# Kernel optimization log

Measured on AMD Instinct MI355X. Metric: run time of the kernel, lower is better.

Reference implementation:

```python
import jax, jax.numpy as jnp
import numpy as np

D_MODEL = 1024; D_STATE = 64; D_CONV = 4; EXPAND = 2; HEADDIM = 128; NGROUPS = 1; CHUNK = 256
D_INNER = EXPAND * D_MODEL            # 2048
NHEADS = D_INNER // HEADDIM           # 16
CONV_DIM = D_INNER + 2 * NGROUPS * D_STATE   # 2176
D_IN_PROJ = 2 * D_INNER + 2 * NGROUPS * D_STATE + NHEADS  # 4240
B = 4; G = 256; L = 2048
EPS = 1e-5


def setup_inputs() -> dict:
    key = jax.random.key(0)
    ks = jax.random.split(key, 12)
    def nrm(k, shape, s=0.02):
        return jax.random.normal(k, shape, jnp.float32) * s
    return dict(
        local_repr=jax.random.normal(ks[0], (B, L, D_MODEL), jnp.float32),
        global_repr=jax.random.normal(ks[1], (B, G, D_MODEL), jnp.float32),
        norm1_w=jnp.ones((D_MODEL,), jnp.float32), norm1_b=jnp.zeros((D_MODEL,), jnp.float32),
        norm2_w=jnp.ones((D_MODEL,), jnp.float32), norm2_b=jnp.zeros((D_MODEL,), jnp.float32),
        norm3_w=jnp.ones((D_MODEL,), jnp.float32), norm3_b=jnp.zeros((D_MODEL,), jnp.float32),
        in_proj_w=nrm(ks[2], (D_IN_PROJ, D_MODEL)),
        conv_w=nrm(ks[3], (CONV_DIM, D_CONV), 0.2),
        conv_b=jnp.zeros((CONV_DIM,), jnp.float32),
        dt_bias=jnp.log(jnp.expm1(jax.random.uniform(ks[4], (NHEADS,), jnp.float32, 1e-3, 0.1))),
        A_log=jnp.log(jax.random.uniform(ks[5], (NHEADS,), jnp.float32, 1.0, 16.0)),
        D_skip=jnp.ones((NHEADS,), jnp.float32),
        ssd_norm_w=jnp.ones((D_INNER,), jnp.float32),
        out_proj_w=nrm(ks[6], (D_MODEL, D_INNER)),
        ffn_w1=nrm(ks[7], (D_MODEL // 2, D_MODEL)),
        ffn_b1=jnp.zeros((D_MODEL // 2,), jnp.float32),
        ffn_w2=nrm(ks[8], (D_MODEL, D_MODEL // 2)),
        ffn_b2=jnp.zeros((D_MODEL,), jnp.float32),
    )


def _ln(x, w, b):
    mu = jnp.mean(x, axis=-1, keepdims=True)
    var = jnp.mean((x - mu) ** 2, axis=-1, keepdims=True)
    return (x - mu) * jax.lax.rsqrt(var + EPS) * w + b


def _segsum(a):
    # a: (..., T) -> (..., T, T) lower-triangular sums a[j+1..i]
    T = a.shape[-1]
    cs = jnp.cumsum(a, axis=-1)
    diff = cs[..., :, None] - cs[..., None, :]
    mask = jnp.tril(jnp.ones((T, T), bool))
    return jnp.where(mask, diff, -jnp.inf)


def _ssd(xdt, a_dt, Bh, Ch):
    # xdt: (b,t,h,p) = x*dt ; a_dt: (b,t,h) = dt*A ; Bh,Ch: (b,t,h,n)
    b, t, h, p = xdt.shape
    n = Bh.shape[-1]
    c = t // CHUNK
    X = xdt.reshape(b, c, CHUNK, h, p)
    Bc = Bh.reshape(b, c, CHUNK, h, n)
    Cc = Ch.reshape(b, c, CHUNK, h, n)
    Ac = a_dt.reshape(b, c, CHUNK, h).transpose(0, 3, 1, 2)  # (b,h,c,k)
    A_cum = jnp.cumsum(Ac, axis=-1)
    Lm = jnp.exp(_segsum(Ac))                                # (b,h,c,k,k)
    Y_diag = jnp.einsum('bckhn,bcshn,bhcks,bcshp->bckhp', Cc, Bc, Lm, X)
    decay_states = jnp.exp(A_cum[..., -1:] - A_cum)          # (b,h,c,k)
    states = jnp.einsum('bckhn,bhck,bckhp->bchpn', Bc, decay_states, X)
    A_last = jnp.pad(A_cum[..., -1], ((0, 0), (0, 0), (1, 0)))
    decay_chunk = jnp.exp(_segsum(A_last))                   # (b,h,c+1,c+1)
    states = jnp.concatenate([jnp.zeros_like(states[:, :1]), states], axis=1)
    new_states = jnp.einsum('bhzc,bchpn->bzhpn', decay_chunk, states)
    states_in = new_states[:, :-1]                           # (b,c,h,p,n)
    out_decay = jnp.exp(A_cum)                               # (b,h,c,k)
    Y_off = jnp.einsum('bckhn,bchpn,bhck->bckhp', Cc, states_in, out_decay)
    return (Y_diag + Y_off).reshape(b, t, h, p)


def _mamba2(x, in_proj_w, conv_w, conv_b, dt_bias, A_log, D_skip, ssd_norm_w, out_proj_w):
    b, t, _ = x.shape
    zxbcdt = x @ in_proj_w.T                                  # (b,t,D_IN_PROJ)
    z = zxbcdt[..., :D_INNER]
    xBC = zxbcdt[..., D_INNER:D_INNER + CONV_DIM]
    dt = jax.nn.softplus(zxbcdt[..., D_INNER + CONV_DIM:] + dt_bias)  # (b,t,h)
    # causal depthwise conv1d, kernel D_CONV
    xp = jnp.pad(xBC, ((0, 0), (D_CONV - 1, 0), (0, 0)))
    xBC = sum(xp[:, i:i + t, :] * conv_w[:, i] for i in range(D_CONV)) + conv_b
    xBC = jax.nn.silu(xBC)
    xs = xBC[..., :D_INNER].reshape(b, t, NHEADS, HEADDIM)
    Bm = xBC[..., D_INNER:D_INNER + NGROUPS * D_STATE].reshape(b, t, NGROUPS, D_STATE)
    Cm = xBC[..., D_INNER + NGROUPS * D_STATE:].reshape(b, t, NGROUPS, D_STATE)
    rep = NHEADS // NGROUPS
    Bh = jnp.repeat(Bm, rep, axis=2)
    Ch = jnp.repeat(Cm, rep, axis=2)
    A = -jnp.exp(A_log)                                       # (h,)
    Y = _ssd(xs * dt[..., None], dt * A, Bh, Ch)
    y = Y + D_skip[None, None, :, None] * xs
    y = y.reshape(b, t, D_INNER)
    # gated RMSNorm (norm_before_gate=False)
    y = y * jax.nn.silu(z)
    y = y * jax.lax.rsqrt(jnp.mean(y * y, axis=-1, keepdims=True) + EPS) * ssd_norm_w
    return y @ out_proj_w.T


def reference(local_repr, global_repr, norm1_w, norm1_b, norm2_w, norm2_b, norm3_w, norm3_b,
              in_proj_w, conv_w, conv_b, dt_bias, A_log, D_skip, ssd_norm_w, out_proj_w,
              ffn_w1, ffn_b1, ffn_w2, ffn_b2):
    local_n = _ln(local_repr, norm1_w, norm1_b)
    global_n = _ln(global_repr, norm2_w, norm2_b)
    x = jnp.concatenate([global_n, local_n], axis=1)          # (B, G+L, D)
    x = _mamba2(x, in_proj_w, conv_w, conv_b, dt_bias, A_log, D_skip, ssd_norm_w, out_proj_w)
    x = x[:, -local_n.shape[1]:, :] + local_n
    x = _ln(x, norm3_w, norm3_b)
    h = jax.nn.gelu(x @ ffn_w1.T + ffn_b1, approximate=False)
    return (h @ ffn_w2.T + ffn_b2) + x
```

## Files before the change

### kernel.cpp

```cpp
#include <hip/hip_runtime.h>
#include <math.h>

#define B_ 4
#define L_ 2048
#define G_ 256
#define T_ 2304
#define DM 1024
#define DINNER 2048
#define NH 16
#define HD 128
#define NSTATE 64
#define CONVD 2176
#define DPROJ 4240
#define NPROJ_PAD 4352
#define NCHUNK 9
#define CK 256
#define EPSV 1e-5f
#define CROWS 16

typedef unsigned short bf16t;
using bf16x8 = __attribute__((ext_vector_type(8))) short;
using f32x4  = __attribute__((ext_vector_type(4))) float;

__device__ __forceinline__ float bf2f(bf16t u) {
  return __uint_as_float(((unsigned int)u) << 16);
}
__device__ __forceinline__ bf16t f2bf(float f) {
  unsigned int u = __float_as_uint(f);
  u += 0x7FFFu + ((u >> 16) & 1u);
  return (bf16t)(u >> 16);
}

__device__ __forceinline__ void g2lds16(const bf16t* g, short* l) {
  __builtin_amdgcn_global_load_lds(
      (const __attribute__((address_space(1))) unsigned int*)g,
      (__attribute__((address_space(3))) unsigned int*)l, 16, 0, 0);
}

__device__ __forceinline__ float2 block_reduce2(float a, float b) {
  __shared__ float sa[4], sb[4];
  #pragma unroll
  for (int off = 32; off > 0; off >>= 1) {
    a += __shfl_down(a, off, 64);
    b += __shfl_down(b, off, 64);
  }
  int lane = threadIdx.x & 63, wid = threadIdx.x >> 6;
  if (lane == 0) { sa[wid] = a; sb[wid] = b; }
  __syncthreads();
  return make_float2(sa[0] + sa[1] + sa[2] + sa[3], sb[0] + sb[1] + sb[2] + sb[3]);
}

__global__ __launch_bounds__(256) void ln_cvt_kernel(
    const float* __restrict__ localr, const float* __restrict__ globalr,
    const float* __restrict__ w1, const float* __restrict__ b1,
    const float* __restrict__ w2, const float* __restrict__ b2,
    bf16t* __restrict__ x, const float* __restrict__ inpw,
    bf16t* __restrict__ inpw_bf) {
  int blk = blockIdx.x;
  if (blk < B_ * T_) {
    int t = blk % T_, b = blk / T_;
    const float *src, *w, *bb;
    if (t < G_) { src = globalr + ((long)b * G_ + t) * DM;        w = w2; bb = b2; }
    else        { src = localr  + ((long)b * L_ + (t - G_)) * DM; w = w1; bb = b1; }
    int d = threadIdx.x * 4;
    float4 v = *(const float4*)&src[d];
    float s = v.x + v.y + v.z + v.w;
    float sq = v.x * v.x + v.y * v.y + v.z * v.z + v.w * v.w;
    float2 r2 = block_reduce2(s, sq);
    float mu = r2.x * (1.f / DM);
    float var = r2.y * (1.f / DM) - mu * mu;
    float rstd = rsqrtf(var + EPSV);
    float4 wv = *(const float4*)&w[d];
    float4 bv = *(const float4*)&bb[d];
    ushort4 o;
    o.x = f2bf((v.x - mu) * rstd * wv.x + bv.x);
    o.y = f2bf((v.y - mu) * rstd * wv.y + bv.y);
    o.z = f2bf((v.z - mu) * rstd * wv.z + bv.z);
    o.w = f2bf((v.w - mu) * rstd * wv.w + bv.w);
    *(ushort4*)&x[(long)blk * DM + d] = o;
  } else {
    long i = (long)(blk - B_ * T_) * 1024 + threadIdx.x * 4;
    const long nreal = (long)DPROJ * DM, ntot = (long)NPROJ_PAD * DM;
    if (i < ntot) {
      ushort4 o = {0, 0, 0, 0};
      if (i < nreal) {
        float4 v = *(const float4*)&inpw[i];
        o.x = f2bf(v.x); o.y = f2bf(v.y); o.z = f2bf(v.z); o.w = f2bf(v.w);
      }
      *(ushort4*)&inpw_bf[i] = o;
    }
  }
}

template<int EPI, bool OFFS>
__global__ __launch_bounds__(256) void gemm_mfma(
    const bf16t* __restrict__ A, const bf16t* __restrict__ W,
    const float* __restrict__ bias, const bf16t* __restrict__ res,
    float* __restrict__ Cf, bf16t* __restrict__ Cb,
    bf16t* __restrict__ z, bf16t* __restrict__ xpre, float* __restrict__ dtr,
    int N, int K) {
  __shared__ __align__(16) short LDS[128 * 136];
  short* As = LDS;
  short* Ws = LDS + 128 * 32;
  int tid = threadIdx.x;
  int lane = tid & 63, w = tid >> 6;
  int wr = w >> 1, wc = w & 1;
  int bm = blockIdx.y * 128, bn = blockIdx.x * 128;
  long bmA = OFFS ? ((long)(bm >> 11) * T_ + G_ + (bm & 2047)) : (long)bm;

  int r1 = tid >> 2,         s1 = (((tid & 3) ^ ((r1 >> 1) & 3))) * 8;
  int r2 = (tid + 256) >> 2, s2 = (((tid & 3) ^ ((r2 >> 1) & 3))) * 8;
  const bf16t* gA1 = A + (bmA + r1) * K + s1;
  const bf16t* gA2 = A + (bmA + r2) * K + s2;
  const bf16t* gW1 = W + (long)(bn + r1) * K + s1;
  const bf16t* gW2 = W + (long)(bn + r2) * K + s2;
  short* lA1 = As + tid * 8;
  short* lA2 = As + (tid + 256) * 8;
  short* lW1 = Ws + tid * 8;
  short* lW2 = Ws + (tid + 256) * 8;

  int arow = wr * 64 + (lane & 15);
  int brow = wc * 64 + (lane & 15);
  int koff = (((lane >> 4) ^ (((lane & 15) >> 1) & 3))) * 8;

  f32x4 acc[4][4] = {};
  for (int k0 = 0; k0 < K; k0 += 32) {
    g2lds16(gA1 + k0, lA1);
    g2lds16(gA2 + k0, lA2);
    g2lds16(gW1 + k0, lW1);
    g2lds16(gW2 + k0, lW2);
    __syncthreads();
    bf16x8 af[4], bf[4];
    #pragma unroll
    for (int mi = 0; mi < 4; mi++) af[mi] = *(bf16x8*)&As[(arow + mi * 16) * 32 + koff];
    #pragma unroll
    for (int ni = 0; ni < 4; ni++) bf[ni] = *(bf16x8*)&Ws[(brow + ni * 16) * 32 + koff];
    #pragma unroll
    for (int mi = 0; mi < 4; mi++)
      #pragma unroll
      for (int ni = 0; ni < 4; ni++)
        acc[mi][ni] = __builtin_amdgcn_mfma_f32_16x16x32_bf16(af[mi], bf[ni], acc[mi][ni], 0, 0, 0);
    __syncthreads();
  }

  int rb = wr * 64 + (lane >> 4) * 4;
  int cb = wc * 64 + (lane & 15);

  if (EPI == 0 && bn >= DINNER + CONVD) {
    #pragma unroll
    for (int mi = 0; mi < 4; mi++)
      #pragma unroll
      for (int ni = 0; ni < 4; ni++)
        #pragma unroll
        for (int r = 0; r < 4; r++) {
          int col = cb + ni * 16;
          if (col < NH)
            dtr[(long)(bm + rb + mi * 16 + r) * NH + col] = acc[mi][ni][r];
        }
    return;
  }

  if (EPI == 3) {
    float* Cs32 = (float*)LDS;
    #pragma unroll
    for (int pass = 0; pass < 2; pass++) {
      __syncthreads();
      if (wr == pass) {
        #pragma unroll
        for (int mi = 0; mi < 4; mi++)
          #pragma unroll
          for (int ni = 0; ni < 4; ni++)
            #pragma unroll
            for (int r = 0; r < 4; r++) {
              int lrow = (lane >> 4) * 4 + mi * 16 + r;
              Cs32[lrow * 136 + cb + ni * 16] = acc[mi][ni][r];
            }
      }
      __syncthreads();
      #pragma unroll
      for (int q = 0; q < 4; q++) {
        int row = q * 16 + (tid >> 4);
        int col = (tid & 15) * 8;
        long grow = bm + pass * 64 + row; int gcol = bn + col;
        float4 v0 = *(float4*)&Cs32[row * 136 + col];
        float4 v1 = *(float4*)&Cs32[row * 136 + col + 4];
        float4 b0 = *(const float4*)&bias[gcol];
        float4 b1 = *(const float4*)&bias[gcol + 4];
        bf16x8 rv = *(const bf16x8*)&res[grow * N + gcol];
        v0.x += b0.x + bf2f((bf16t)rv[0]); v0.y += b0.y + bf2f((bf16t)rv[1]);
        v0.z += b0.z + bf2f((bf16t)rv[2]); v0.w += b0.w + bf2f((bf16t)rv[3]);
        v1.x += b1.x + bf2f((bf16t)rv[4]); v1.y += b1.y + bf2f((bf16t)rv[5]);
        v1.z += b1.z + bf2f((bf16t)rv[6]); v1.w += b1.w + bf2f((bf16t)rv[7]);
        *(float4*)&Cf[grow * N + gcol] = v0;
        *(float4*)&Cf[grow * N + gcol + 4] = v1;
      }
    }
    return;
  }

  __syncthreads();
  bf16t* Cs = (bf16t*)LDS;
  #pragma unroll
  for (int mi = 0; mi < 4; mi++)
    #pragma unroll
    for (int ni = 0; ni < 4; ni++)
      #pragma unroll
      for (int r = 0; r < 4; r++) {
        float v = acc[mi][ni][r];
        if (EPI == 2) {
          v += bias[bn + cb + ni * 16];
          v = 0.5f * v * (1.f + erff(v * 0.70710678118f));
        }
        Cs[(rb + mi * 16 + r) * 136 + cb + ni * 16] = f2bf(v);
      }
  __syncthreads();
  #pragma unroll
  for (int pass = 0; pass < 8; pass++) {
    int row = pass * 16 + (tid >> 4);
    int col = (tid & 15) * 8;
    bf16x8 vv = *(bf16x8*)&Cs[row * 136 + col];
    long grow = bm + row; int gcol = bn + col;
    if (EPI == 0) {
      if (bn < DINNER) *(bf16x8*)&z[grow * DINNER + gcol] = vv;
      else             *(bf16x8*)&xpre[grow * CONVD + (gcol - DINNER)] = vv;
    } else {
      *(bf16x8*)&Cb[grow * N + gcol] = vv;
    }
  }
}

__global__ __launch_bounds__(256) void cumsum_kernel(
    const float* __restrict__ dtraw, const float* __restrict__ dt_bias,
    const float* __restrict__ A_log, float* __restrict__ dt,
    float* __restrict__ Acum) {
  int bid = blockIdx.x;
  int c = bid % NCHUNK; int hh = bid / NCHUNK;
  int h = hh % NH; int b = hh / NH;
  int k = threadIdx.x;
  float a = -__expf(A_log[h]);
  long t = (long)b * T_ + c * CK + k;
  float v0 = dtraw[t * NH + h] + dt_bias[h];
  float dtv = (v0 > 20.f) ? v0 : log1pf(__expf(v0));
  dt[t * NH + h] = dtv;
  float v = dtv * a;
  __shared__ float buf[2][CK];
  int cur = 0;
  buf[0][k] = v; __syncthreads();
  for (int off = 1; off < CK; off <<= 1) {
    float tv = buf[cur][k];
    if (k >= off) tv += buf[cur][k - off];
    buf[1 - cur][k] = tv; cur ^= 1; __syncthreads();
  }
  Acum[(long)bid * CK + k] = buf[cur][k];
}

__global__ __launch_bounds__(256) void conv_kernel(
    const bf16t* __restrict__ xpre, const float* __restrict__ cw,
    const float* __restrict__ cb, bf16t* __restrict__ out) {
  int gt = blockIdx.x * 256 + threadIdx.x;
  int cg = gt % 272; int rt = gt / 272;
  int c0 = cg * 8;
  long r0 = (long)rt * CROWS;
  int t0 = (int)(r0 % T_);

  float wreg[4][8];
  #pragma unroll
  for (int j = 0; j < 8; j++) {
    float4 wa = *(const float4*)&cw[(c0 + j) * 4];
    wreg[0][j] = wa.x; wreg[1][j] = wa.y; wreg[2][j] = wa.z; wreg[3][j] = wa.w;
  }
  float4 cb0 = *(const float4*)&cb[c0];
  float4 cb1 = *(const float4*)&cb[c0 + 4];
  float bias[8] = {cb0.x, cb0.y, cb0.z, cb0.w, cb1.x, cb1.y, cb1.z, cb1.w};

  bf16x8 win[4];
  #pragma unroll
  for (int i = 0; i < 3; i++) {
    if (t0 - 3 + i >= 0) win[i] = *(const bf16x8*)&xpre[(r0 - 3 + i) * CONVD + c0];
    else                 win[i] = bf16x8{0,0,0,0,0,0,0,0};
  }

  #pragma unroll
  for (int k = 0; k < CROWS; k++) {
    win[3] = *(const bf16x8*)&xpre[(r0 + k) * CONVD + c0];
    float acc[8];
    #pragma unroll
    for (int j = 0; j < 8; j++) acc[j] = bias[j];
    #pragma unroll
    for (int i = 0; i < 4; i++)
      #pragma unroll
      for (int j = 0; j < 8; j++)
        acc[j] += bf2f((bf16t)win[i][j]) * wreg[i][j];
    bf16x8 o;
    #pragma unroll
    for (int j = 0; j < 8; j++) {
      float s = acc[j] / (1.f + __expf(-acc[j]));
      o[j] = (short)f2bf(s);
    }
    *(bf16x8*)&out[(r0 + k) * CONVD + c0] = o;
    win[0] = win[1]; win[1] = win[2]; win[2] = win[3];
  }
}

__global__ __launch_bounds__(256) void chunk_states_kernel(
    const bf16t* __restrict__ xbc, const float* __restrict__ dt,
    const float* __restrict__ Acum, float* __restrict__ cs) {
  int bid = blockIdx.x;
  int h = bid & 15; int bc = bid >> 4;
  int c = bc & 7; int b = bc >> 3;
  int tid = threadIdx.x;
  int lane = tid & 63, w = tid >> 6;
  long tch = (long)b * T_ + c * CK;
  int acb = ((b * NH + h) * NCHUNK + c) * CK;
  float Alast = Acum[acb + CK - 1];

  __shared__ bf16t Xt[128][72];
  __shared__ bf16t Bt[64][72];
  __shared__ float wk[64];

  f32x4 acc[8] = {};
  for (int kb = 0; kb < 4; kb++) {
    int s0 = kb * 64;
    __syncthreads();
    if (tid < 64)
      wk[tid] = __expf(Alast - Acum[acb + s0 + tid]) * dt[(tch + s0 + tid) * NH + h];
    __syncthreads();
    for (int e = tid; e < 64 * 32; e += 256) {
      int s = e & 63, p4 = e >> 6;
      ushort4 u = *(const ushort4*)&xbc[(tch + s0 + s) * CONVD + h * HD + p4 * 4];
      float wv = wk[s];
      Xt[p4 * 4 + 0][s] = f2bf(bf2f(u.x) * wv);
      Xt[p4 * 4 + 1][s] = f2bf(bf2f(u.y) * wv);
      Xt[p4 * 4 + 2][s] = f2bf(bf2f(u.z) * wv);
      Xt[p4 * 4 + 3][s] = f2bf(bf2f(u.w) * wv);
    }
    for (int e = tid; e < 64 * 16; e += 256) {
      int s = e & 63, n4 = e >> 6;
      ushort4 u = *(const ushort4*)&xbc[(tch + s0 + s) * CONVD + DINNER + n4 * 4];
      Bt[n4 * 4 + 0][s] = u.x; Bt[n4 * 4 + 1][s] = u.y;
      Bt[n4 * 4 + 2][s] = u.z; Bt[n4 * 4 + 3][s] = u.w;
    }
    __syncthreads();
    #pragma unroll
    for (int ks = 0; ks < 2; ks++) {
      int koff = (lane >> 4) * 8 + ks * 32;
      bf16x8 bfr = *(bf16x8*)&Bt[w * 16 + (lane & 15)][koff];
      #pragma unroll
      for (int mi = 0; mi < 8; mi++) {
        bf16x8 af = *(bf16x8*)&Xt[mi * 16 + (lane & 15)][koff];
        acc[mi] = __builtin_amdgcn_mfma_f32_16x16x32_bf16(af, bfr, acc[mi], 0, 0, 0);
      }
    }
  }
  int cbid = (b * NCHUNK + c) * NH + h;
  float* out = cs + (long)cbid * HD * NSTATE;
  int n = w * 16 + (lane & 15);
  #pragma unroll
  for (int mi = 0; mi < 8; mi++) {
    #pragma unroll
    for (int r = 0; r < 4; r++) {
      int p = mi * 16 + (lane >> 4) * 4 + r;
      out[p * NSTATE + n] = acc[mi][r];
    }
  }
}

__global__ __launch_bounds__(256) void state_pass_kernel(
    float* __restrict__ cs, const float* __restrict__ Acum) {
  int bh = blockIdx.x;
  int b = bh / NH, h = bh % NH;
  int e0 = blockIdx.y * 1024 + threadIdx.x;
  for (int q = 0; q < 4; q++) {
    int e = e0 + q * 256;
    float s = 0.f;
    for (int c = 0; c < NCHUNK; c++) {
      long idx = ((long)(b * NCHUNK + c) * NH + h) * (HD * NSTATE) + e;
      if (c < NCHUNK - 1) {
        float tmp = cs[idx];
        cs[idx] = s;
        float g = __expf(Acum[((b * NH + h) * NCHUNK + c) * CK + CK - 1]);
        s = s * g + tmp;
      } else {
        cs[idx] = s;
      }
    }
  }
}

__global__ __launch_bounds__(256) void ssd_y_kernel(
    const bf16t* __restrict__ xbc, const float* __restrict__ dt,
    const float* __restrict__ Acum, const float* __restrict__ sin_,
    const float* __restrict__ Dskip, bf16t* __restrict__ Y) {
  int bid = blockIdx.x;
  int h = bid & 15; int bc = bid >> 4;
  int c = 1 + (bc & 7); int b = bc >> 3;
  int rt = blockIdx.y;
  int tid = threadIdx.x;
  int lane = tid & 63, w = tid >> 6;
  int wr = w >> 1, wc = w & 1;
  long tch = (long)b * T_ + c * CK;
  long tbase = tch + rt * 128;
  int acb = ((b * NH + h) * NCHUNK + c) * CK;

  __shared__ bf16t Cs[128][72];
  __shared__ bf16t Bs[64][72];
  __shared__ bf16t Xt[128][72];
  __shared__ bf16t Sm[128][72];
  __shared__ float Akl[128];
  __shared__ float Asl[64];
  __shared__ float dts[64];

  for (int e = tid; e < 128 * 8; e += 256) {
    int row = e >> 3, seg = (e & 7) * 8;
    *(bf16x8*)&Cs[row][seg] =
        *(const bf16x8*)&xbc[(tbase + row) * CONVD + DINNER + NSTATE + seg];
  }
  if (tid < 128) Akl[tid] = Acum[acb + rt * 128 + tid];

  f32x4 acc[4][4] = {};
  int nsb = 2 * (rt + 1);
  for (int sb = 0; sb < nsb; sb++) {
    int s0 = sb * 64;
    __syncthreads();
    if (tid < 64) {
      Asl[tid] = Acum[acb + s0 + tid];
      dts[tid] = dt[(tch + s0 + tid) * NH + h];
    }
    __syncthreads();
    for (int e = tid; e < 64 * 8; e += 256) {
      int row = e >> 3, seg = (e & 7) * 8;
      *(bf16x8*)&Bs[row][seg] =
          *(const bf16x8*)&xbc[(tch + s0 + row) * CONVD + DINNER + seg];
    }
    for (int e = tid; e < 64 * 32; e += 256) {
      int s = e & 63, p4 = e >> 6;
      ushort4 u = *(const ushort4*)&xbc[(tch + s0 + s) * CONVD + h * HD + p4 * 4];
      float dtv = dts[s];
      Xt[p4 * 4 + 0][s] = f2bf(bf2f(u.x) * dtv);
      Xt[p4 * 4 + 1][s] = f2bf(bf2f(u.y) * dtv);
      Xt[p4 * 4 + 2][s] = f2bf(bf2f(u.z) * dtv);
      Xt[p4 * 4 + 3][s] = f2bf(bf2f(u.w) * dtv);
    }
    __syncthreads();
    {
      f32x4 sacc[2][4] = {};
      int rw0 = w * 32;
      #pragma unroll
      for (int ks = 0; ks < 2; ks++) {
        int koff = (lane >> 4) * 8 + ks * 32;
        bf16x8 a0 = *(bf16x8*)&Cs[rw0 + (lane & 15)][koff];
        bf16x8 a1 = *(bf16x8*)&Cs[rw0 + 16 + (lane & 15)][koff];
        #pragma unroll
        for (int ni = 0; ni < 4; ni++) {
          bf16x8 bfr = *(bf16x8*)&Bs[ni * 16 + (lane & 15)][koff];
          sacc[0][ni] = __builtin_amdgcn_mfma_f32_16x16x32_bf16(a0, bfr, sacc[0][ni], 0, 0, 0);
          sacc[1][ni] = __builtin_amdgcn_mfma_f32_16x16x32_bf16(a1, bfr, sacc[1][ni], 0, 0, 0);
        }
      }
      #pragma unroll
      for (int mi = 0; mi < 2; mi++) {
        #pragma unroll
        for (int ni = 0; ni < 4; ni++) {
          #pragma unroll
          for (int r = 0; r < 4; r++) {
            int row = rw0 + mi * 16 + (lane >> 4) * 4 + r;
            int scol = ni * 16 + (lane & 15);
            int kglob = rt * 128 + row;
            int sglob = s0 + scol;
            float val = 0.f;
            if (sglob <= kglob) val = sacc[mi][ni][r] * __expf(Akl[row] - Asl[scol]);
            Sm[row][scol] = f2bf(val);
          }
        }
      }
    }
    __syncthreads();
    #pragma unroll
    for (int ks = 0; ks < 2; ks++) {
      int koff = (lane >> 4) * 8 + ks * 32;
      bf16x8 af[4], bfr[4];
      #pragma unroll
      for (int mi = 0; mi < 4; mi++) af[mi] = *(bf16x8*)&Sm[wr * 64 + mi * 16 + (lane & 15)][koff];
      #pragma unroll
      for (int ni = 0; ni < 4; ni++) bfr[ni] = *(bf16x8*)&Xt[wc * 64 + ni * 16 + (lane & 15)][koff];
      #pragma unroll
      for (int mi = 0; mi < 4; mi++)
        #pragma unroll
        for (int ni = 0; ni < 4; ni++)
          acc[mi][ni] = __builtin_amdgcn_mfma_f32_16x16x32_bf16(af[mi], bfr[ni], acc[mi][ni], 0, 0, 0);
    }
  }

  float ekr[16];
  #pragma unroll
  for (int mi = 0; mi < 4; mi++)
    #pragma unroll
    for (int r = 0; r < 4; r++)
      ekr[mi * 4 + r] = __expf(Akl[wr * 64 + mi * 16 + (lane >> 4) * 4 + r]);

  int cbid = (b * NCHUNK + c) * NH + h;
  const float* sinb = sin_ + (long)cbid * HD * NSTATE;
  #pragma unroll
  for (int ni = 0; ni < 4; ni++) {
    f32x4 offacc[4] = {};
    int p = wc * 64 + ni * 16 + (lane & 15);
    #pragma unroll
    for (int ks = 0; ks < 2; ks++) {
      int koff = (lane >> 4) * 8 + ks * 32;
      const float* srow = sinb + p * NSTATE + koff;
      float4 sa = *(const float4*)srow;
      float4 sbv = *(const float4*)(srow + 4);
      bf16x8 bfr;
      bfr[0] = (short)f2bf(sa.x);  bfr[1] = (short)f2bf(sa.y);
      bfr[2] = (short)f2bf(sa.z);  bfr[3] = (short)f2bf(sa.w);
      bfr[4] = (short)f2bf(sbv.x); bfr[5] = (short)f2bf(sbv.y);
      bfr[6] = (short)f2bf(sbv.z); bfr[7] = (short)f2bf(sbv.w);
      #pragma unroll
      for (int mi = 0; mi < 4; mi++) {
        bf16x8 af = *(bf16x8*)&Cs[wr * 64 + mi * 16 + (lane & 15)][koff];
        offacc[mi] = __builtin_amdgcn_mfma_f32_16x16x32_bf16(af, bfr, offacc[mi], 0, 0, 0);
      }
    }
    #pragma unroll
    for (int mi = 0; mi < 4; mi++)
      #pragma unroll
      for (int r = 0; r < 4; r++)
        acc[mi][ni][r] += ekr[mi * 4 + r] * offacc[mi][r];
  }

  float dsk = Dskip[h];
  #pragma unroll
  for (int mi = 0; mi < 4; mi++) {
    #pragma unroll
    for (int r = 0; r < 4; r++) {
      int row = wr * 64 + mi * 16 + (lane >> 4) * 4 + r;
      long t = tbase + row;
      #pragma unroll
      for (int ni = 0; ni < 4; ni++) {
        int p = wc * 64 + ni * 16 + (lane & 15);
        float xsv = bf2f(xbc[t * CONVD + h * HD + p]);
        Y[t * DINNER + h * HD + p] = f2bf(acc[mi][ni][r] + dsk * xsv);
      }
    }
  }
}

__global__ __launch_bounds__(256) void gate_rms_cvt_kernel(
    const bf16t* __restrict__ z, const float* __restrict__ nw,
    bf16t* __restrict__ Y,
    const float* __restrict__ outw, const float* __restrict__ f1w,
    const float* __restrict__ f2w, bf16t* __restrict__ o_out,
    bf16t* __restrict__ o_f1, bf16t* __restrict__ o_f2) {
  int blk = blockIdx.x;
  if (blk < B_ * L_) {
    long r = (long)(blk >> 11) * T_ + G_ + (blk & 2047);
    const bf16t* zrow = z + r * DINNER;
    bf16t* yrow = Y + r * DINNER;
    int tid = threadIdx.x;
    float v[8]; float sq = 0.f;
    #pragma unroll
    for (int i = 0; i < 4; i++) {
      int d = tid * 2 + 512 * i;
      ushort2 zu = *(const ushort2*)&zrow[d];
      ushort2 yu = *(const ushort2*)&yrow[d];
      float z0 = bf2f(zu.x), z1 = bf2f(zu.y);
      float y0 = bf2f(yu.x) * (z0 / (1.f + __expf(-z0)));
      float y1 = bf2f(yu.y) * (z1 / (1.f + __expf(-z1)));
      v[2 * i] = y0; v[2 * i + 1] = y1;
      sq += y0 * y0 + y1 * y1;
    }
    float2 r2 = block_reduce2(sq, 0.f);
    float rms = rsqrtf(r2.x * (1.f / DINNER) + EPSV);
    #pragma unroll
    for (int i = 0; i < 4; i++) {
      int d = tid * 2 + 512 * i;
      ushort2 o;
      o.x = f2bf(v[2 * i] * rms * nw[d]);
      o.y = f2bf(v[2 * i + 1] * rms * nw[d + 1]);
      *(ushort2*)&yrow[d] = o;
    }
  } else {
    long i = (long)(blk - B_ * L_) * 1024 + threadIdx.x * 4;
    const long n1 = (long)DM * DINNER;
    const long n2 = (long)(DM / 2) * DM;
    const float* src; bf16t* dst; long off;
    if (i < n1) { src = outw; dst = o_out; off = i; }
    else if (i < n1 + n2) { src = f1w; dst = o_f1; off = i - n1; }
    else { src = f2w; dst = o_f2; off = i - n1 - n2; }
    float4 v = *(const float4*)&src[off];
    ushort4 o;
    o.x = f2bf(v.x); o.y = f2bf(v.y); o.z = f2bf(v.z); o.w = f2bf(v.w);
    *(ushort4*)&dst[off] = o;
  }
}

__global__ __launch_bounds__(256) void res_ln3_kernel(
    const bf16t* __restrict__ mfull, const bf16t* __restrict__ x,
    const float* __restrict__ w3, const float* __restrict__ b3,
    bf16t* __restrict__ x2) {
  int rl = blockIdx.x;
  int tl = rl & 2047, b = rl >> 11;
  long rt = (long)b * T_ + G_ + tl;
  const bf16t* m = mfull + (long)rl * DM;
  const bf16t* xr = x + rt * DM;
  int tid = threadIdx.x;
  float v[4]; float s = 0.f, sq = 0.f;
  #pragma unroll
  for (int i = 0; i < 2; i++) {
    int d = tid * 2 + 512 * i;
    ushort2 mu2 = *(const ushort2*)&m[d];
    ushort2 xu2 = *(const ushort2*)&xr[d];
    float a0 = bf2f(mu2.x) + bf2f(xu2.x);
    float a1 = bf2f(mu2.y) + bf2f(xu2.y);
    v[2 * i] = a0; v[2 * i + 1] = a1;
    s += a0 + a1; sq += a0 * a0 + a1 * a1;
  }
  float2 r2 = block_reduce2(s, sq);
  float mu = r2.x * (1.f / DM);
  float var = r2.y * (1.f / DM) - mu * mu;
  float rstd = rsqrtf(var + EPSV);
  bf16t* dst = x2 + (long)rl * DM;
  #pragma unroll
  for (int i = 0; i < 2; i++) {
    int d = tid * 2 + 512 * i;
    ushort2 o;
    o.x = f2bf((v[2 * i] - mu) * rstd * w3[d] + b3[d]);
    o.y = f2bf((v[2 * i + 1] - mu) * rstd * w3[d + 1] + b3[d + 1]);
    *(ushort2*)&dst[d] = o;
  }
}

extern "C" void kernel_launch(void* const* d_in, const int* in_sizes, int n_in,
                              void* d_out, int out_size, void* d_ws, size_t ws_size,
                              hipStream_t stream) {
  const float* localr = (const float*)d_in[0];
  const float* globalr= (const float*)d_in[1];
  const float* n1w = (const float*)d_in[2];
  const float* n1b = (const float*)d_in[3];
  const float* n2w = (const float*)d_in[4];
  const float* n2b = (const float*)d_in[5];
  const float* n3w = (const float*)d_in[6];
  const float* n3b = (const float*)d_in[7];
  const float* inpw= (const float*)d_in[8];
  const float* convw=(const float*)d_in[9];
  const float* convb=(const float*)d_in[10];
  const float* dtb = (const float*)d_in[11];
  const float* alog= (const float*)d_in[12];
  const float* dskp= (const float*)d_in[13];
  const float* ssdw= (const float*)d_in[14];
  const float* outw= (const float*)d_in[15];
  const float* f1w = (const float*)d_in[16];
  const float* f1b = (const float*)d_in[17];
  const float* f2w = (const float*)d_in[18];
  const float* f2b = (const float*)d_in[19];

  char* ws = (char*)d_ws;
  bf16t* x     = (bf16t*)(ws + 0);
  bf16t* z     = (bf16t*)(ws + 18874368);
  bf16t* mfull = (bf16t*)(ws + 18874368);
  bf16t* xpre  = (bf16t*)(ws + 56623104);
  bf16t* Yb    = (bf16t*)(ws + 56623104);
  float* dtraw = (float*)(ws + 96731136);
  float* dt    = (float*)(ws + 97320960);
  float* Acum  = (float*)(ws + 97910784);
  bf16t* xbc   = (bf16t*)(ws + 98500608);
  bf16t* x2bf  = (bf16t*)(ws + 98500608);
  bf16t* hbuf  = (bf16t*)(ws + 115277824);
  bf16t* outw_bf = (bf16t*)(ws + 123666432);
  bf16t* f1w_bf  = (bf16t*)(ws + 127860736);
  bf16t* f2w_bf  = (bf16t*)(ws + 128909312);
  float* cs    = (float*)(ws + 138608640);
  bf16t* inpw_bf = (bf16t*)(ws + 138608640);

  ln_cvt_kernel<<<B_ * T_ + 4352, 256, 0, stream>>>(
      localr, globalr, n1w, n1b, n2w, n2b, x, inpw, inpw_bf);

  gemm_mfma<0, false><<<dim3(NPROJ_PAD / 128, (B_ * T_) / 128), 256, 0, stream>>>(
      x, inpw_bf, nullptr, nullptr, nullptr, nullptr, z, xpre, dtraw, NPROJ_PAD, DM);

  cumsum_kernel<<<B_ * NH * NCHUNK, 256, 0, stream>>>(dtraw, dtb, alog, dt, Acum);

  conv_kernel<<<(B_ * T_ / CROWS) * 272 / 256, 256, 0, stream>>>(xpre, convw, convb, xbc);

  chunk_states_kernel<<<B_ * (NCHUNK - 1) * NH, 256, 0, stream>>>(xbc, dt, Acum, cs);

  state_pass_kernel<<<dim3(B_ * NH, 8), 256, 0, stream>>>(cs, Acum);

  ssd_y_kernel<<<dim3(B_ * (NCHUNK - 1) * NH, 2), 256, 0, stream>>>(
      xbc, dt, Acum, cs, dskp, Yb);

  gate_rms_cvt_kernel<<<B_ * L_ + 3072, 256, 0, stream>>>(
      z, ssdw, Yb, outw, f1w, f2w, outw_bf, f1w_bf, f2w_bf);

  gemm_mfma<1, true><<<dim3(DM / 128, (B_ * L_) / 128), 256, 0, stream>>>(
      Yb, outw_bf, nullptr, nullptr, nullptr, mfull, nullptr, nullptr, nullptr,
      DM, DINNER);

  res_ln3_kernel<<<B_ * L_, 256, 0, stream>>>(mfull, x, n3w, n3b, x2bf);

  gemm_mfma<2, false><<<dim3((DM / 2) / 128, (B_ * L_) / 128), 256, 0, stream>>>(
      x2bf, f1w_bf, f1b, nullptr, nullptr, hbuf, nullptr, nullptr, nullptr,
      DM / 2, DM);

  gemm_mfma<3, false><<<dim3(DM / 128, (B_ * L_) / 128), 256, 0, stream>>>(
      hbuf, f2w_bf, f2b, x2bf, (float*)d_out, nullptr, nullptr, nullptr, nullptr,
      DM, DM / 2);
}
```

Before: 527.9 us.

## Add dedicated 256x256 double-buffered MFMA GEMM for the input projection

Replaces the generic 128x128 GEMM used for the input projection with a specialised kernel. It uses 256x256 tiles, 512 threads, a swizzled double-buffered LDS layout, staged async global-to-LDS loads interleaved with MFMA phases, and setprio hints. The larger tile raises arithmetic intensity and overlaps loads with compute. The cost is 128KB of LDS per block, fewer blocks, and extra complexity in the dt-column and epilogue handling. The EPI==0 path is removed from the generic kernel.

```diff
diff --git a/kernel.cpp b/kernel.cpp
--- a/kernel.cpp
+++ b/kernel.cpp
@@ -92,6 +92,168 @@
   }
 }
 
+__global__ __launch_bounds__(512, 2) void gemm_inproj(
+    const bf16t* __restrict__ A, const bf16t* __restrict__ W,
+    bf16t* __restrict__ z, bf16t* __restrict__ xpre, float* __restrict__ dtr) {
+  __shared__ short LDS8[65536];
+  int tid = threadIdx.x;
+  int lane = tid & 63, w = tid >> 6;
+  int wm = w >> 2, wn = w & 3;
+  int l15 = lane & 15;
+  int bn = blockIdx.x * 256, bm = blockIdx.y * 256;
+
+  int csub = ((lane & 7) ^ (lane >> 3)) * 8;
+  const bf16t* srcA = A + (long)(bm + w * 16 + (lane >> 3)) * 1024 + csub;
+  const bf16t* srcW = W + (long)(bn + w * 16 + (lane >> 3)) * 1024 + csub;
+  int stageDst = w * 1024 + lane * 8;
+
+  int aoff0 = l15 * 64 + (((lane >> 4) + 0) ^ (lane & 7)) * 8;
+  int aoff1 = l15 * 64 + (((lane >> 4) + 4) ^ (lane & 7)) * 8;
+  int boff0 = ((wn & 1) * 64 + l15) * 64 + (((lane >> 4) + 0) ^ (lane & 7)) * 8;
+  int boff1 = ((wn & 1) * 64 + l15) * 64 + (((lane >> 4) + 4) ^ (lane & 7)) * 8;
+  int aBase0 = wm * 8192;
+  int bBase0 = 16384 + (wn >> 1) * 8192;
+
+  f32x4 acc[8][4] = {};
+  bf16x8 af[4][2], bq[4][2];
+
+#define STAGE2(gsrc, ldsoff) do { \
+    g2lds16((gsrc), LDS8 + (ldsoff) + stageDst); \
+    g2lds16((gsrc) + 8 * 1024, LDS8 + (ldsoff) + stageDst + 512); } while (0)
+
+  STAGE2(srcA, 0);
+  STAGE2(srcA + 128 * 1024, 8192);
+  STAGE2(srcW, 16384);
+  STAGE2(srcW + 128 * 1024, 24576);
+  STAGE2(srcW + 64, 32768 + 16384);
+  STAGE2(srcW + 128 * 1024 + 64, 32768 + 24576);
+  asm volatile("s_waitcnt vmcnt(4)" ::: "memory");
+  __builtin_amdgcn_s_barrier();
+
+  const int nt = 16;
+  #pragma unroll 2
+  for (int t = 0; t < nt; ++t) {
+    int cs_ = (t & 1) * 32768;
+    int ns_ = 32768 - cs_;
+    const short* aB = LDS8 + cs_ + aBase0;
+    const short* bB = LDS8 + cs_ + bBase0;
+
+    #pragma unroll
+    for (int mi = 0; mi < 4; mi++) {
+      af[mi][0] = *(const bf16x8*)&aB[mi * 1024 + aoff0];
+      af[mi][1] = *(const bf16x8*)&aB[mi * 1024 + aoff1];
+    }
+    #pragma unroll
+    for (int ni = 0; ni < 2; ni++) {
+      bq[ni][0] = *(const bf16x8*)&bB[ni * 1024 + boff0];
+      bq[ni][1] = *(const bf16x8*)&bB[ni * 1024 + boff1];
+    }
+    if (t + 1 < nt) STAGE2(srcA + (t + 1) * 64, ns_);
+    __builtin_amdgcn_s_barrier();
+    __builtin_amdgcn_s_setprio(1);
+    #pragma unroll
+    for (int ks = 0; ks < 2; ks++)
+      #pragma unroll
+      for (int mi = 0; mi < 4; mi++)
+        #pragma unroll
+        for (int ni = 0; ni < 2; ni++)
+          acc[mi][ni] = __builtin_amdgcn_mfma_f32_16x16x32_bf16(af[mi][ks], bq[ni][ks], acc[mi][ni], 0, 0, 0);
+    __builtin_amdgcn_s_setprio(0);
+    __builtin_amdgcn_s_barrier();
+
+    #pragma unroll
+    for (int ni = 2; ni < 4; ni++) {
+      bq[ni][0] = *(const bf16x8*)&bB[ni * 1024 + boff0];
+      bq[ni][1] = *(const bf16x8*)&bB[ni * 1024 + boff1];
+    }
+    if (t + 1 < nt) STAGE2(srcA + 128 * 1024 + (t + 1) * 64, ns_ + 8192);
+    __builtin_amdgcn_s_barrier();
+    __builtin_amdgcn_s_setprio(1);
+    #pragma unroll
+    for (int ks = 0; ks < 2; ks++)
+      #pragma unroll
+      for (int mi = 0; mi < 4; mi++)
+        #pragma unroll
+        for (int ni = 2; ni < 4; ni++)
+          acc[mi][ni] = __builtin_amdgcn_mfma_f32_16x16x32_bf16(af[mi][ks], bq[ni][ks], acc[mi][ni], 0, 0, 0);
+    __builtin_amdgcn_s_setprio(0);
+    __builtin_amdgcn_s_barrier();
+
+    #pragma unroll
+    for (int mi = 0; mi < 4; mi++) {
+      af[mi][0] = *(const bf16x8*)&aB[(mi + 4) * 1024 + aoff0];
+      af[mi][1] = *(const bf16x8*)&aB[(mi + 4) * 1024 + aoff1];
+    }
+    if (t + 2 < nt) STAGE2(srcW + (t + 2) * 64, cs_ + 16384);
+    __builtin_amdgcn_s_barrier();
+    __builtin_amdgcn_s_setprio(1);
+    #pragma unroll
+    for (int ks = 0; ks < 2; ks++)
+      #pragma unroll
+      for (int mi = 0; mi < 4; mi++)
+        #pragma unroll
+        for (int ni = 2; ni < 4; ni++)
+          acc[mi + 4][ni] = __builtin_amdgcn_mfma_f32_16x16x32_bf16(af[mi][ks], bq[ni][ks], acc[mi + 4][ni], 0, 0, 0);
+    __builtin_amdgcn_s_setprio(0);
+    __builtin_amdgcn_s_barrier();
+
+    if (t + 2 < nt) STAGE2(srcW + 128 * 1024 + (t + 2) * 64, cs_ + 24576);
+    __builtin_amdgcn_s_barrier();
+    __builtin_amdgcn_s_setprio(1);
+    #pragma unroll
+    for (int ks = 0; ks < 2; ks++)
+      #pragma unroll
+      for (int mi = 0; mi < 4; mi++)
+        #pragma unroll
+        for (int ni = 0; ni < 2; ni++)
+          acc[mi + 4][ni] = __builtin_amdgcn_mfma_f32_16x16x32_bf16(af[mi][ks], bq[ni][ks], acc[mi + 4][ni], 0, 0, 0);
+    __builtin_amdgcn_s_setprio(0);
+    if (t + 2 < nt)      asm volatile("s_waitcnt vmcnt(4)" ::: "memory");
+    else if (t + 1 < nt) asm volatile("s_waitcnt vmcnt(0)" ::: "memory");
+    __builtin_amdgcn_s_barrier();
+  }
+#undef STAGE2
+
+  if (bn == 4096 && wn == 2) {
+    #pragma unroll
+    for (int mi = 0; mi < 8; mi++)
+      #pragma unroll
+      for (int r = 0; r < 4; r++) {
+        int row = bm + wm * 128 + mi * 16 + (lane >> 4) * 4 + r;
+        dtr[(long)row * NH + l15] = acc[mi][0][r];
+      }
+  }
+
+  bf16t* Cs = (bf16t*)LDS8;
+  #pragma unroll
+  for (int pass = 0; pass < 2; pass++) {
+    __syncthreads();
+    if (wm == pass) {
+      #pragma unroll
+      for (int mi = 0; mi < 8; mi++)
+        #pragma unroll
+        for (int ni = 0; ni < 4; ni++)
+          #pragma unroll
+          for (int r = 0; r < 4; r++)
+            Cs[(mi * 16 + (lane >> 4) * 4 + r) * 264 + wn * 64 + ni * 16 + l15] =
+                f2bf(acc[mi][ni][r]);
+    }
+    __syncthreads();
+    #pragma unroll
+    for (int q = 0; q < 8; q++) {
+      int idx = q * 512 + tid;
+      int row = idx >> 5, cg = idx & 31;
+      int gcol = bn + cg * 8;
+      long grow = bm + pass * 128 + row;
+      if (gcol < DINNER + CONVD) {
+        bf16x8 v = *(bf16x8*)&Cs[row * 264 + cg * 8];
+        if (gcol < DINNER) *(bf16x8*)&z[grow * DINNER + gcol] = v;
+        else               *(bf16x8*)&xpre[grow * CONVD + (gcol - DINNER)] = v;
+      }
+    }
+  }
+}
+
 template<int EPI, bool OFFS>
 __global__ __launch_bounds__(256) void gemm_mfma(
     const bf16t* __restrict__ A, const bf16t* __restrict__ W,
@@ -146,20 +308,6 @@
   int rb = wr * 64 + (lane >> 4) * 4;
   int cb = wc * 64 + (lane & 15);
 
-  if (EPI == 0 && bn >= DINNER + CONVD) {
-    #pragma unroll
-    for (int mi = 0; mi < 4; mi++)
-      #pragma unroll
-      for (int ni = 0; ni < 4; ni++)
-        #pragma unroll
-        for (int r = 0; r < 4; r++) {
-          int col = cb + ni * 16;
-          if (col < NH)
-            dtr[(long)(bm + rb + mi * 16 + r) * NH + col] = acc[mi][ni][r];
-        }
-    return;
-  }
-
   if (EPI == 3) {
     float* Cs32 = (float*)LDS;
     #pragma unroll
@@ -220,12 +368,7 @@
     int col = (tid & 15) * 8;
     bf16x8 vv = *(bf16x8*)&Cs[row * 136 + col];
     long grow = bm + row; int gcol = bn + col;
-    if (EPI == 0) {
-      if (bn < DINNER) *(bf16x8*)&z[grow * DINNER + gcol] = vv;
-      else             *(bf16x8*)&xpre[grow * CONVD + (gcol - DINNER)] = vv;
-    } else {
-      *(bf16x8*)&Cb[grow * N + gcol] = vv;
-    }
+    *(bf16x8*)&Cb[grow * N + gcol] = vv;
   }
 }
 
@@ -675,8 +818,8 @@
   ln_cvt_kernel<<<B_ * T_ + 4352, 256, 0, stream>>>(
       localr, globalr, n1w, n1b, n2w, n2b, x, inpw, inpw_bf);
 
-  gemm_mfma<0, false><<<dim3(NPROJ_PAD / 128, (B_ * T_) / 128), 256, 0, stream>>>(
-      x, inpw_bf, nullptr, nullptr, nullptr, nullptr, z, xpre, dtraw, NPROJ_PAD, DM);
+  gemm_inproj<<<dim3(NPROJ_PAD / 256, (B_ * T_) / 256), 512, 0, stream>>>(
+      x, inpw_bf, z, xpre, dtraw);
 
   cumsum_kernel<<<B_ * NH * NCHUNK, 256, 0, stream>>>(dtraw, dtb, alog, dt, Acum);
 
```

After: 501.3 us. -5.0%, faster.
